# Kernel tuning notes

Hardware: AMD Instinct MI355X
Metric: run time of the kernel (lower is better)

Reference implementation:

```python
import jax, jax.numpy as jnp
import numpy as np

LN_EPS = 1e-5
N_NODES = 50000
IN_DIM = 128
OUT_DIM = 128
N_EDGES = 800000


def _ln(x, g, b):
    m = jnp.mean(x, axis=-1, keepdims=True)
    v = jnp.mean((x - m) ** 2, axis=-1, keepdims=True)
    return (x - m) * jax.lax.rsqrt(v + LN_EPS) * g + b


def setup_inputs() -> dict:
    key = jax.random.key(0)
    ks = jax.random.split(key, 16)

    def lin(k, fan_in, fan_out):
        return jax.random.normal(k, (fan_in, fan_out), dtype=jnp.float32) / np.sqrt(fan_in)

    x = jax.random.normal(ks[0], (N_NODES, IN_DIM), dtype=jnp.float32)
    edge_index = jax.random.randint(ks[1], (2, N_EDGES), 0, N_NODES, dtype=jnp.int64)
    return {
        "x": x,
        "edge_index": edge_index,
        # transform: Linear(in,out) + LayerNorm
        "W1": lin(ks[2], IN_DIM, OUT_DIM), "b1": jnp.zeros((OUT_DIM,), jnp.float32),
        "g1": jnp.ones((OUT_DIM,), jnp.float32), "bt1": jnp.zeros((OUT_DIM,), jnp.float32),
        # edge_attention: Linear(2*out,out) -> ReLU -> Linear(out,1) -> Sigmoid
        "We1": lin(ks[3], 2 * OUT_DIM, OUT_DIM), "be1": jnp.zeros((OUT_DIM,), jnp.float32),
        "We2": lin(ks[4], OUT_DIM, 1), "be2": jnp.zeros((1,), jnp.float32),
        # node_attention: Linear(out,out) -> ReLU -> Linear(out,1) -> Sigmoid (computed, unused)
        "Wn1": lin(ks[5], OUT_DIM, OUT_DIM), "bn1": jnp.zeros((OUT_DIM,), jnp.float32),
        "Wn2": lin(ks[6], OUT_DIM, 1), "bn2": jnp.zeros((1,), jnp.float32),
        # update_gate: Linear(2*out,out) -> Sigmoid
        "Wg": lin(ks[7], 2 * OUT_DIM, OUT_DIM), "bg": jnp.zeros((OUT_DIM,), jnp.float32),
        # final LayerNorm
        "g2": jnp.ones((OUT_DIM,), jnp.float32), "bt2": jnp.zeros((OUT_DIM,), jnp.float32),
    }


def reference(x, edge_index, W1, b1, g1, bt1, We1, be1, We2, be2,
              Wn1, bn1, Wn2, bn2, Wg, bg, g2, bt2):
    n = x.shape[0]
    # transform: Linear -> LayerNorm -> ReLU (Dropout is identity in eval)
    h = jax.nn.relu(_ln(x @ W1 + b1, g1, bt1))           # [N, D]
    row, col = edge_index[0], edge_index[1]
    h_src = h[row]                                        # [E, D]
    ef = jnp.concatenate([h_src, h[col]], axis=1)         # [E, 2D]
    edge_weights = jax.nn.sigmoid(jax.nn.relu(ef @ We1 + be1) @ We2 + be2)[:, 0]  # [E]
    # node_weights computed in original forward but never used in the output
    node_weights = jax.nn.sigmoid(jax.nn.relu(h @ Wn1 + bn1) @ Wn2 + bn2)[:, 0]
    _ = node_weights
    # weighted scatter-add: aggr[dst] += edge_weights[i] * h[src]
    aggr = jax.ops.segment_sum(edge_weights[:, None] * h_src, col, num_segments=n)  # [N, D]
    gate = jax.nn.sigmoid(jnp.concatenate([h, aggr], axis=-1) @ Wg + bg)
    h_new = gate * aggr + (1.0 - gate) * h
    return _ln(h_new, g2, bt2)
```

## Files before the change

kernel.cpp:

```cpp
#include <hip/hip_runtime.h>
#include <math.h>

#define D 128
#define NT 32
#define AGT 16
#define LP 132
#define SCB 64
#define HB 256

__device__ __forceinline__ float wave_allsum(float v) {
    #pragma unroll
    for (int off = 32; off; off >>= 1) v += __shfl_xor(v, off);
    return v;
}

__global__ void __launch_bounds__(256) fused_hist_transform(
    const int* __restrict__ ei, int* __restrict__ deg, int E,
    const float* __restrict__ x, const float* __restrict__ W1, const float* __restrict__ b1,
    const float* __restrict__ g1, const float* __restrict__ bt1,
    const float* __restrict__ We1, const float* __restrict__ be1,
    float* __restrict__ AH, float* __restrict__ B, int N)
{
    if (blockIdx.x < HB) {
        for (int e = blockIdx.x * 256 + threadIdx.x; e < E; e += HB * 256)
            atomicAdd(&deg[ei[E + e]], 1);
        return;
    }
    __shared__ float xs[NT][LP];
    const int t = threadIdx.x;
    const int q = t >> 6, lane = t & 63;
    const int cg = (lane & 31) * 4;
    const int kh = (lane >> 5) * 64;
    const int khi = lane >> 5;
    const int base = (blockIdx.x - HB) * NT;

    {
        int node = t >> 3, c0 = (t & 7) * 16;
        int gn = min(base + node, N - 1);
        const float4* src = (const float4*)(x + (size_t)gn * D + c0);
        float4* dst = (float4*)&xs[node][c0];
        dst[0] = src[0]; dst[1] = src[1]; dst[2] = src[2]; dst[3] = src[3];
    }

    float4 acc[8];
    #pragma unroll
    for (int n = 0; n < 8; ++n) acc[n] = make_float4(0.f,0.f,0.f,0.f);
    for (int k4 = 0; k4 < 16; ++k4) {
        int k = kh + k4 * 4;
        float4 w0 = *(const float4*)&W1[(k+0) * 128 + cg];
        float4 w1 = *(const float4*)&W1[(k+1) * 128 + cg];
        float4 w2 = *(const float4*)&W1[(k+2) * 128 + cg];
        float4 w3 = *(const float4*)&W1[(k+3) * 128 + cg];
        #pragma unroll
        for (int n = 0; n < 8; ++n) {
            float4 xv = *(const float4*)&xs[q*8+n][k];
            acc[n].x += xv.x*w0.x + xv.y*w1.x + xv.z*w2.x + xv.w*w3.x;
            acc[n].y += xv.x*w0.y + xv.y*w1.y + xv.z*w2.y + xv.w*w3.y;
            acc[n].z += xv.x*w0.z + xv.y*w1.z + xv.z*w2.z + xv.w*w3.z;
            acc[n].w += xv.x*w0.w + xv.y*w1.w + xv.z*w2.w + xv.w*w3.w;
        }
    }
    #pragma unroll
    for (int n = 0; n < 8; ++n) {
        acc[n].x += __shfl_xor(acc[n].x, 32);
        acc[n].y += __shfl_xor(acc[n].y, 32);
        acc[n].z += __shfl_xor(acc[n].z, 32);
        acc[n].w += __shfl_xor(acc[n].w, 32);
    }

    {
        float4 b4 = *(const float4*)&b1[cg];
        float4 g4 = *(const float4*)&g1[cg];
        float4 t4 = *(const float4*)&bt1[cg];
        #pragma unroll
        for (int n = 0; n < 8; ++n) {
            int node = q * 8 + n;
            float v0 = acc[n].x + b4.x, v1 = acc[n].y + b4.y;
            float v2 = acc[n].z + b4.z, v3 = acc[n].w + b4.w;
            float s  = wave_allsum(v0 + v1 + v2 + v3) * 0.5f;
            float qq = wave_allsum(v0*v0 + v1*v1 + v2*v2 + v3*v3) * 0.5f;
            float m = s * (1.f/128.f);
            float var = qq * (1.f/128.f) - m*m;
            float rs = rsqrtf(var + 1e-5f);
            float4 h4;
            h4.x = fmaxf((v0 - m)*rs*g4.x + t4.x, 0.f);
            h4.y = fmaxf((v1 - m)*rs*g4.y + t4.y, 0.f);
            h4.z = fmaxf((v2 - m)*rs*g4.z + t4.z, 0.f);
            h4.w = fmaxf((v3 - m)*rs*g4.w + t4.w, 0.f);
            if (khi == 0) {
                *(float4*)&xs[node][cg] = h4;
                int gn = base + node;
                if (gn < N) *(float4*)&AH[(size_t)gn * 256 + 128 + cg] = h4;
            }
        }
    }

    float4 aA[8], aB[8];
    #pragma unroll
    for (int n = 0; n < 8; ++n) { aA[n] = make_float4(0.f,0.f,0.f,0.f); aB[n] = make_float4(0.f,0.f,0.f,0.f); }
    for (int k4 = 0; k4 < 16; ++k4) {
        int k = kh + k4 * 4;
        float4 t0 = *(const float4*)&We1[(k+0) * 128 + cg];
        float4 t1 = *(const float4*)&We1[(k+1) * 128 + cg];
        float4 t2 = *(const float4*)&We1[(k+2) * 128 + cg];
        float4 t3 = *(const float4*)&We1[(k+3) * 128 + cg];
        float4 u0 = *(const float4*)&We1[(k+128) * 128 + cg];
        float4 u1 = *(const float4*)&We1[(k+129) * 128 + cg];
        float4 u2 = *(const float4*)&We1[(k+130) * 128 + cg];
        float4 u3 = *(const float4*)&We1[(k+131) * 128 + cg];
        #pragma unroll
        for (int n = 0; n < 8; ++n) {
            float4 hv = *(const float4*)&xs[q*8+n][k];
            aA[n].x += hv.x*t0.x + hv.y*t1.x + hv.z*t2.x + hv.w*t3.x;
            aA[n].y += hv.x*t0.y + hv.y*t1.y + hv.z*t2.y + hv.w*t3.y;
            aA[n].z += hv.x*t0.z + hv.y*t1.z + hv.z*t2.z + hv.w*t3.z;
            aA[n].w += hv.x*t0.w + hv.y*t1.w + hv.z*t2.w + hv.w*t3.w;
            aB[n].x += hv.x*u0.x + hv.y*u1.x + hv.z*u2.x + hv.w*u3.x;
            aB[n].y += hv.x*u0.y + hv.y*u1.y + hv.z*u2.y + hv.w*u3.y;
            aB[n].z += hv.x*u0.z + hv.y*u1.z + hv.z*u2.z + hv.w*u3.z;
            aB[n].w += hv.x*u0.w + hv.y*u1.w + hv.z*u2.w + hv.w*u3.w;
        }
    }
    {
        float4 be4 = *(const float4*)&be1[cg];
        #pragma unroll
        for (int n = 0; n < 8; ++n) {
            aA[n].x += __shfl_xor(aA[n].x, 32);
            aA[n].y += __shfl_xor(aA[n].y, 32);
            aA[n].z += __shfl_xor(aA[n].z, 32);
            aA[n].w += __shfl_xor(aA[n].w, 32);
            aB[n].x += __shfl_xor(aB[n].x, 32);
            aB[n].y += __shfl_xor(aB[n].y, 32);
            aB[n].z += __shfl_xor(aB[n].z, 32);
            aB[n].w += __shfl_xor(aB[n].w, 32);
            int gn = base + q*8 + n;
            if (khi == 0 && gn < N) {
                float4 a4 = make_float4(aA[n].x + be4.x, aA[n].y + be4.y,
                                        aA[n].z + be4.z, aA[n].w + be4.w);
                *(float4*)&AH[(size_t)gn * 256 + cg] = a4;
                *(float4*)&B[(size_t)gn * D + cg]    = aB[n];
            }
        }
    }
}

__global__ void __launch_bounds__(256) scan_a(const int* __restrict__ deg,
                                              int* __restrict__ bsum, int N) {
    __shared__ int red[256];
    const int b = blockIdx.x, t = threadIdx.x;
    const int C = (N + SCB - 1) / SCB;
    const int W = (C + 255) / 256;
    int s0 = b * C + t * W;
    int s1 = min(s0 + W, min((b + 1) * C, N));
    int s = 0;
    for (int i = s0; i < s1; ++i) s += deg[i];
    red[t] = s;
    __syncthreads();
    #pragma unroll
    for (int d = 128; d; d >>= 1) {
        if (t < d) red[t] += red[t + d];
        __syncthreads();
    }
    if (t == 0) bsum[b] = red[0];
}

__global__ void __launch_bounds__(256) scan_c(const int* __restrict__ deg,
                                              const int* __restrict__ bsum,
                                              int* __restrict__ off,
                                              int* __restrict__ cursor, int N) {
    __shared__ int pre[256];
    __shared__ int bofs;
    const int b = blockIdx.x, t = threadIdx.x;
    const int C = (N + SCB - 1) / SCB;
    const int W = (C + 255) / 256;
    if (t == 0) {
        int r = 0;
        for (int i = 0; i < b; ++i) r += bsum[i];
        bofs = r;
        if (b == SCB - 1) off[N] = r + bsum[b];
    }
    int s0 = b * C + t * W;
    int s1 = min(s0 + W, min((b + 1) * C, N));
    int s = 0;
    for (int i = s0; i < s1; ++i) s += deg[i];
    pre[t] = s;
    __syncthreads();
    for (int d = 1; d < 256; d <<= 1) {
        int vv = (t >= d) ? pre[t - d] : 0;
        __syncthreads();
        if (t >= d) pre[t] += vv;
        __syncthreads();
    }
    int run = bofs + ((t == 0) ? 0 : pre[t - 1]);
    for (int i = s0; i < s1; ++i) {
        off[i] = run;
        cursor[i] = run;
        run += deg[i];
    }
}

__global__ void __launch_bounds__(256) scatter_kernel(const int* __restrict__ ei,
                                                      int* __restrict__ cursor,
                                                      int* __restrict__ ssrc, int E) {
    int e = blockIdx.x * 256 + threadIdx.x;
    if (e < E) {
        int pos = atomicAdd(&cursor[ei[E + e]], 1);
        ssrc[pos] = ei[e];
    }
}

__global__ void __launch_bounds__(256) aggate(
    const int* __restrict__ off, const int* __restrict__ ssrc,
    const float* __restrict__ AH, const float* __restrict__ B,
    const float* __restrict__ We2, const float* __restrict__ be2,
    const float* __restrict__ Wg, const float* __restrict__ bg,
    const float* __restrict__ g2, const float* __restrict__ bt2,
    float* __restrict__ out, int N)
{
    __shared__ float hs[AGT][LP];
    __shared__ float ag[AGT][LP];
    const int t = threadIdx.x;
    const int q = t >> 6, lane = t & 63;
    const int g = lane >> 4;
    const int c8 = (lane & 15) * 8;
    const int base = blockIdx.x * AGT;

    {
        int node = t >> 4, c0 = (t & 15) * 8;
        size_t gofs = (size_t)min(base + node, N - 1) * 256 + 128 + c0;
        const float4* src = (const float4*)(AH + gofs);
        float4* dst = (float4*)&hs[node][c0];
        dst[0] = src[0]; dst[1] = src[1];
    }

    {
        const float4* Wp = (const float4*)(We2 + c8);
        float4 w0 = Wp[0], w1 = Wp[1];
        const float be = be2[0];

        for (int n = 0; n < 4; ++n) {
            int node = base + q * 4 + n;
            float4 acc0 = make_float4(0.f,0.f,0.f,0.f);
            float4 acc1 = make_float4(0.f,0.f,0.f,0.f);
            if (node < N) {
                const int s = off[node], e = off[node + 1];
                const int deg = e - s;
                if (deg > 0) {
                    const float4* Bp = (const float4*)(B + (size_t)node * D + c8);
                    float4 b0 = Bp[0], b1 = Bp[1];
                    if (deg <= 64) {
                        int myidx = ssrc[min(s + lane, e - 1)];
                        const int nit = (deg + 7) >> 3;
                        for (int it = 0; it < nit; ++it) {
                            int ja = it * 8 + g * 2;
                            int jb = ja + 1;
                            int sa = __shfl(myidx, min(ja, deg - 1));
                            int sb = __shfl(myidx, min(jb, deg - 1));
                            const float4* Ra = (const float4*)(AH + (size_t)sa * 256 + c8);
                            const float4* Rb = (const float4*)(AH + (size_t)sb * 256 + c8);
                            float4 aa0 = Ra[0], aa1 = Ra[1];
                            float4 ha0 = Ra[32], ha1 = Ra[33];
                            float4 ab0 = Rb[0], ab1 = Rb[1];
                            float4 hb0 = Rb[32], hb1 = Rb[33];
                            float da = fmaxf(aa0.x + b0.x, 0.f) * w0.x + fmaxf(aa0.y + b0.y, 0.f) * w0.y
                                     + fmaxf(aa0.z + b0.z, 0.f) * w0.z + fmaxf(aa0.w + b0.w, 0.f) * w0.w
                                     + fmaxf(aa1.x + b1.x, 0.f) * w1.x + fmaxf(aa1.y + b1.y, 0.f) * w1.y
                                     + fmaxf(aa1.z + b1.z, 0.f) * w1.z + fmaxf(aa1.w + b1.w, 0.f) * w1.w;
                            float db = fmaxf(ab0.x + b0.x, 0.f) * w0.x + fmaxf(ab0.y + b0.y, 0.f) * w0.y
                                     + fmaxf(ab0.z + b0.z, 0.f) * w0.z + fmaxf(ab0.w + b0.w, 0.f) * w0.w
                                     + fmaxf(ab1.x + b1.x, 0.f) * w1.x + fmaxf(ab1.y + b1.y, 0.f) * w1.y
                                     + fmaxf(ab1.z + b1.z, 0.f) * w1.z + fmaxf(ab1.w + b1.w, 0.f) * w1.w;
                            da += __shfl_xor(da, 1);  db += __shfl_xor(db, 1);
                            da += __shfl_xor(da, 2);  db += __shfl_xor(db, 2);
                            da += __shfl_xor(da, 4);  db += __shfl_xor(db, 4);
                            da += __shfl_xor(da, 8);  db += __shfl_xor(db, 8);
                            float wa = (ja < deg) ? 1.f / (1.f + expf(-(da + be))) : 0.f;
                            float wb = (jb < deg) ? 1.f / (1.f + expf(-(db + be))) : 0.f;
                            acc0.x += wa * ha0.x + wb * hb0.x; acc0.y += wa * ha0.y + wb * hb0.y;
                            acc0.z += wa * ha0.z + wb * hb0.z; acc0.w += wa * ha0.w + wb * hb0.w;
                            acc1.x += wa * ha1.x + wb * hb1.x; acc1.y += wa * ha1.y + wb * hb1.y;
                            acc1.z += wa * ha1.z + wb * hb1.z; acc1.w += wa * ha1.w + wb * hb1.w;
                        }
                    } else {
                        const int nit = (deg + 7) >> 3;
                        for (int it = 0; it < nit; ++it) {
                            int ja = s + it * 8 + g * 2;
                            int jb = ja + 1;
                            int sa = ssrc[min(ja, e - 1)];
                            int sb = ssrc[min(jb, e - 1)];
                            const float4* Ra = (const float4*)(AH + (size_t)sa * 256 + c8);
                            const float4* Rb = (const float4*)(AH + (size_t)sb * 256 + c8);
                            float4 aa0 = Ra[0], aa1 = Ra[1];
                            float4 ha0 = Ra[32], ha1 = Ra[33];
                            float4 ab0 = Rb[0], ab1 = Rb[1];
                            float4 hb0 = Rb[32], hb1 = Rb[33];
                            float da = fmaxf(aa0.x + b0.x, 0.f) * w0.x + fmaxf(aa0.y + b0.y, 0.f) * w0.y
                                     + fmaxf(aa0.z + b0.z, 0.f) * w0.z + fmaxf(aa0.w + b0.w, 0.f) * w0.w
                                     + fmaxf(aa1.x + b1.x, 0.f) * w1.x + fmaxf(aa1.y + b1.y, 0.f) * w1.y
                                     + fmaxf(aa1.z + b1.z, 0.f) * w1.z + fmaxf(aa1.w + b1.w, 0.f) * w1.w;
                            float db = fmaxf(ab0.x + b0.x, 0.f) * w0.x + fmaxf(ab0.y + b0.y, 0.f) * w0.y
                                     + fmaxf(ab0.z + b0.z, 0.f) * w0.z + fmaxf(ab0.w + b0.w, 0.f) * w0.w
                                     + fmaxf(ab1.x + b1.x, 0.f) * w1.x + fmaxf(ab1.y + b1.y, 0.f) * w1.y
                                     + fmaxf(ab1.z + b1.z, 0.f) * w1.z + fmaxf(ab1.w + b1.w, 0.f) * w1.w;
                            da += __shfl_xor(da, 1);  db += __shfl_xor(db, 1);
                            da += __shfl_xor(da, 2);  db += __shfl_xor(db, 2);
                            da += __shfl_xor(da, 4);  db += __shfl_xor(db, 4);
                            da += __shfl_xor(da, 8);  db += __shfl_xor(db, 8);
                            float wa = (ja < e) ? 1.f / (1.f + expf(-(da + be))) : 0.f;
                            float wb = (jb < e) ? 1.f / (1.f + expf(-(db + be))) : 0.f;
                            acc0.x += wa * ha0.x + wb * hb0.x; acc0.y += wa * ha0.y + wb * hb0.y;
                            acc0.z += wa * ha0.z + wb * hb0.z; acc0.w += wa * ha0.w + wb * hb0.w;
                            acc1.x += wa * ha1.x + wb * hb1.x; acc1.y += wa * ha1.y + wb * hb1.y;
                            acc1.z += wa * ha1.z + wb * hb1.z; acc1.w += wa * ha1.w + wb * hb1.w;
                        }
                    }
                    #pragma unroll
                    for (int o = 16; o <= 32; o <<= 1) {
                        acc0.x += __shfl_xor(acc0.x, o); acc0.y += __shfl_xor(acc0.y, o);
                        acc0.z += __shfl_xor(acc0.z, o); acc0.w += __shfl_xor(acc0.w, o);
                        acc1.x += __shfl_xor(acc1.x, o); acc1.y += __shfl_xor(acc1.y, o);
                        acc1.z += __shfl_xor(acc1.z, o); acc1.w += __shfl_xor(acc1.w, o);
                    }
                }
            }
            if (g == 0) {
                *(float4*)&ag[q*4+n][c8]     = acc0;
                *(float4*)&ag[q*4+n][c8 + 4] = acc1;
            }
        }
    }

    {
        const int cg = (lane & 31) * 4;
        const int kh = (lane >> 5) * 64;
        const int khi = lane >> 5;

        float4 acc[4];
        #pragma unroll
        for (int n = 0; n < 4; ++n) acc[n] = make_float4(0.f,0.f,0.f,0.f);
        for (int k4 = 0; k4 < 16; ++k4) {
            int k = kh + k4 * 4;
            float4 w0 = *(const float4*)&Wg[(k+0) * 128 + cg];
            float4 w1 = *(const float4*)&Wg[(k+1) * 128 + cg];
            float4 w2 = *(const float4*)&Wg[(k+2) * 128 + cg];
            float4 w3 = *(const float4*)&Wg[(k+3) * 128 + cg];
            float4 u0 = *(const float4*)&Wg[(k+128) * 128 + cg];
            float4 u1 = *(const float4*)&Wg[(k+129) * 128 + cg];
            float4 u2 = *(const float4*)&Wg[(k+130) * 128 + cg];
            float4 u3 = *(const float4*)&Wg[(k+131) * 128 + cg];
            #pragma unroll
            for (int n = 0; n < 4; ++n) {
                float4 v = *(const float4*)&hs[q*4+n][k];
                float4 a = *(const float4*)&ag[q*4+n][k];
                acc[n].x += v.x*w0.x + v.y*w1.x + v.z*w2.x + v.w*w3.x
                          + a.x*u0.x + a.y*u1.x + a.z*u2.x + a.w*u3.x;
                acc[n].y += v.x*w0.y + v.y*w1.y + v.z*w2.y + v.w*w3.y
                          + a.x*u0.y + a.y*u1.y + a.z*u2.y + a.w*u3.y;
                acc[n].z += v.x*w0.z + v.y*w1.z + v.z*w2.z + v.w*w3.z
                          + a.x*u0.z + a.y*u1.z + a.z*u2.z + a.w*u3.z;
                acc[n].w += v.x*w0.w + v.y*w1.w + v.z*w2.w + v.w*w3.w
                          + a.x*u0.w + a.y*u1.w + a.z*u2.w + a.w*u3.w;
            }
        }
        #pragma unroll
        for (int n = 0; n < 4; ++n) {
            acc[n].x += __shfl_xor(acc[n].x, 32);
            acc[n].y += __shfl_xor(acc[n].y, 32);
            acc[n].z += __shfl_xor(acc[n].z, 32);
            acc[n].w += __shfl_xor(acc[n].w, 32);
        }

        float4 bg4 = *(const float4*)&bg[cg];
        float4 gg4 = *(const float4*)&g2[cg];
        float4 bb4 = *(const float4*)&bt2[cg];
        #pragma unroll
        for (int n = 0; n < 4; ++n) {
            int node = q*4 + n;
            float4 av = *(const float4*)&ag[node][cg];
            float4 hv = *(const float4*)&hs[node][cg];
            float g0 = 1.f / (1.f + expf(-(acc[n].x + bg4.x)));
            float g1v = 1.f / (1.f + expf(-(acc[n].y + bg4.y)));
            float g2v = 1.f / (1.f + expf(-(acc[n].z + bg4.z)));
            float g3 = 1.f / (1.f + expf(-(acc[n].w + bg4.w)));
            float y0 = g0 * av.x + (1.f - g0) * hv.x;
            float y1 = g1v * av.y + (1.f - g1v) * hv.y;
            float y2 = g2v * av.z + (1.f - g2v) * hv.z;
            float y3 = g3 * av.w + (1.f - g3) * hv.w;
            float s  = wave_allsum(y0 + y1 + y2 + y3) * 0.5f;
            float qq = wave_allsum(y0*y0 + y1*y1 + y2*y2 + y3*y3) * 0.5f;
            float m = s * (1.f/128.f);
            float var = qq * (1.f/128.f) - m*m;
            float rs = rsqrtf(var + 1e-5f);
            int gn = base + node;
            if (khi == 0 && gn < N) {
                float4 o4;
                o4.x = (y0 - m)*rs*gg4.x + bb4.x;
                o4.y = (y1 - m)*rs*gg4.y + bb4.y;
                o4.z = (y2 - m)*rs*gg4.z + bb4.z;
                o4.w = (y3 - m)*rs*gg4.w + bb4.w;
                *(float4*)&out[(size_t)gn * D + cg] = o4;
            }
        }
    }
}

extern "C" void kernel_launch(void* const* d_in, const int* in_sizes, int n_in,
                              void* d_out, int out_size, void* d_ws, size_t ws_size,
                              hipStream_t stream) {
    const float* x   = (const float*)d_in[0];
    const int*   ei  = (const int*)d_in[1];
    const float* W1  = (const float*)d_in[2];
    const float* b1  = (const float*)d_in[3];
    const float* g1  = (const float*)d_in[4];
    const float* bt1 = (const float*)d_in[5];
    const float* We1 = (const float*)d_in[6];
    const float* be1 = (const float*)d_in[7];
    const float* We2 = (const float*)d_in[8];
    const float* be2 = (const float*)d_in[9];
    const float* Wg  = (const float*)d_in[14];
    const float* bg  = (const float*)d_in[15];
    const float* g2  = (const float*)d_in[16];
    const float* bt2 = (const float*)d_in[17];

    const int N = in_sizes[0] / D;
    const int E = in_sizes[1] / 2;
    const size_t ND = (size_t)N * D;

    float* AH   = (float*)d_ws;
    float* B    = AH + 2 * ND;
    int* deg    = (int*)(B + ND);
    int* off    = deg + (N + 1);
    int* cursor = off + (N + 1);
    int* ssrc   = cursor + (N + 1);
    int* bsum   = ssrc + E;

    (void)hipMemsetAsync(deg, 0, (size_t)(N + 1) * sizeof(int), stream);

    const int nblkT = (N + NT - 1) / NT;
    fused_hist_transform<<<HB + nblkT, 256, 0, stream>>>(
        ei, deg, E, x, W1, b1, g1, bt1, We1, be1, AH, B, N);
    scan_a<<<SCB, 256, 0, stream>>>(deg, bsum, N);
    scan_c<<<SCB, 256, 0, stream>>>(deg, bsum, off, cursor, N);
    scatter_kernel<<<(E + 255) / 256, 256, 0, stream>>>(ei, cursor, ssrc, E);
    aggate<<<(N + AGT - 1) / AGT, 256, 0, stream>>>(off, ssrc, AH, B, We2, be2,
                                                    Wg, bg, g2, bt2, (float*)d_out, N);
}
```

Baseline: 335.1 us.

## Fuse CSR build into transform kernel using in-kernel grid barriers

Merges the degree histogram, the two-pass scan and the edge scatter into the first 64 blocks of the transform kernel, synchronized by atomic counter spin barriers. This removes three kernel launches and lets CSR construction overlap with the dense transform work running in the other blocks. The cost is fewer blocks (64 instead of 256) doing the histogram and scatter atomics, plus spin-wait barriers. Those barriers assume all 64 CSR blocks are co-resident, which holds because they have the lowest block indices.

```diff
diff --git a/kernel.cpp b/kernel.cpp
--- a/kernel.cpp
+++ b/kernel.cpp
@@ -5,8 +5,7 @@
 #define NT 32
 #define AGT 16
 #define LP 132
-#define SCB 64
-#define HB 256
+#define CSB 64
 
 __device__ __forceinline__ float wave_allsum(float v) {
     #pragma unroll
@@ -14,25 +13,95 @@
     return v;
 }
 
-__global__ void __launch_bounds__(256) fused_hist_transform(
-    const int* __restrict__ ei, int* __restrict__ deg, int E,
+__global__ void __launch_bounds__(256) fused_csr_transform(
+    const int* __restrict__ ei, int* __restrict__ deg, int* __restrict__ ctr,
+    int* __restrict__ bsum, int* __restrict__ off, int* __restrict__ cursor,
+    int* __restrict__ ssrc, int E,
     const float* __restrict__ x, const float* __restrict__ W1, const float* __restrict__ b1,
     const float* __restrict__ g1, const float* __restrict__ bt1,
     const float* __restrict__ We1, const float* __restrict__ be1,
     float* __restrict__ AH, float* __restrict__ B, int N)
 {
-    if (blockIdx.x < HB) {
-        for (int e = blockIdx.x * 256 + threadIdx.x; e < E; e += HB * 256)
+    if (blockIdx.x < CSB) {
+        __shared__ int red[256];
+        __shared__ int bofs;
+        const int b = blockIdx.x, t = threadIdx.x;
+
+        for (int e = b * 256 + t; e < E; e += CSB * 256)
             atomicAdd(&deg[ei[E + e]], 1);
+        __threadfence();
+        __syncthreads();
+        if (t == 0) {
+            atomicAdd(&ctr[0], 1);
+            while (atomicAdd(&ctr[0], 0) < CSB) __builtin_amdgcn_s_sleep(2);
+        }
+        __syncthreads();
+
+        const int C = (N + CSB - 1) / CSB;
+        const int W = (C + 255) / 256;
+        int s0 = b * C + t * W;
+        int s1 = min(s0 + W, min((b + 1) * C, N));
+        int s = 0;
+        for (int i = s0; i < s1; ++i) s += atomicAdd(&deg[i], 0);
+        red[t] = s;
+        __syncthreads();
+        #pragma unroll
+        for (int d = 128; d; d >>= 1) {
+            if (t < d) red[t] += red[t + d];
+            __syncthreads();
+        }
+        if (t == 0) atomicExch(&bsum[b], red[0]);
+        __threadfence();
+        __syncthreads();
+        if (t == 0) {
+            atomicAdd(&ctr[1], 1);
+            while (atomicAdd(&ctr[1], 0) < CSB) __builtin_amdgcn_s_sleep(2);
+        }
+        __syncthreads();
+
+        if (t == 0) {
+            int r = 0;
+            for (int i = 0; i < b; ++i) r += atomicAdd(&bsum[i], 0);
+            bofs = r;
+            if (b == CSB - 1) atomicExch(&off[N], r + atomicAdd(&bsum[b], 0));
+        }
+        red[t] = s;
+        __syncthreads();
+        for (int d = 1; d < 256; d <<= 1) {
+            int vv = (t >= d) ? red[t - d] : 0;
+            __syncthreads();
+            if (t >= d) red[t] += vv;
+            __syncthreads();
+        }
+        int run = bofs + ((t == 0) ? 0 : red[t - 1]);
+        for (int i = s0; i < s1; ++i) {
+            int dv = atomicAdd(&deg[i], 0);
+            atomicExch(&off[i], run);
+            atomicExch(&cursor[i], run);
+            run += dv;
+        }
+        __threadfence();
+        __syncthreads();
+        if (t == 0) {
+            atomicAdd(&ctr[2], 1);
+            while (atomicAdd(&ctr[2], 0) < CSB) __builtin_amdgcn_s_sleep(2);
+        }
+        __syncthreads();
+
+        for (int e = b * 256 + t; e < E; e += CSB * 256) {
+            int pos = atomicAdd(&cursor[ei[E + e]], 1);
+            ssrc[pos] = ei[e];
+        }
         return;
     }
+
     __shared__ float xs[NT][LP];
     const int t = threadIdx.x;
     const int q = t >> 6, lane = t & 63;
     const int cg = (lane & 31) * 4;
     const int kh = (lane >> 5) * 64;
     const int khi = lane >> 5;
-    const int base = (blockIdx.x - HB) * NT;
+    const int base = (blockIdx.x - CSB) * NT;
 
     {
         int node = t >> 3, c0 = (t & 7) * 16;
@@ -141,71 +210,6 @@
                 *(float4*)&B[(size_t)gn * D + cg]    = aB[n];
             }
         }
-    }
-}
-
-__global__ void __launch_bounds__(256) scan_a(const int* __restrict__ deg,
-                                              int* __restrict__ bsum, int N) {
-    __shared__ int red[256];
-    const int b = blockIdx.x, t = threadIdx.x;
-    const int C = (N + SCB - 1) / SCB;
-    const int W = (C + 255) / 256;
-    int s0 = b * C + t * W;
-    int s1 = min(s0 + W, min((b + 1) * C, N));
-    int s = 0;
-    for (int i = s0; i < s1; ++i) s += deg[i];
-    red[t] = s;
-    __syncthreads();
-    #pragma unroll
-    for (int d = 128; d; d >>= 1) {
-        if (t < d) red[t] += red[t + d];
-        __syncthreads();
-    }
-    if (t == 0) bsum[b] = red[0];
-}
-
-__global__ void __launch_bounds__(256) scan_c(const int* __restrict__ deg,
-                                              const int* __restrict__ bsum,
-                                              int* __restrict__ off,
-                                              int* __restrict__ cursor, int N) {
-    __shared__ int pre[256];
-    __shared__ int bofs;
-    const int b = blockIdx.x, t = threadIdx.x;
-    const int C = (N + SCB - 1) / SCB;
-    const int W = (C + 255) / 256;
-    if (t == 0) {
-        int r = 0;
-        for (int i = 0; i < b; ++i) r += bsum[i];
-        bofs = r;
-        if (b == SCB - 1) off[N] = r + bsum[b];
-    }
-    int s0 = b * C + t * W;
-    int s1 = min(s0 + W, min((b + 1) * C, N));
-    int s = 0;
-    for (int i = s0; i < s1; ++i) s += deg[i];
-    pre[t] = s;
-    __syncthreads();
-    for (int d = 1; d < 256; d <<= 1) {
-        int vv = (t >= d) ? pre[t - d] : 0;
-        __syncthreads();
-        if (t >= d) pre[t] += vv;
-        __syncthreads();
-    }
-    int run = bofs + ((t == 0) ? 0 : pre[t - 1]);
-    for (int i = s0; i < s1; ++i) {
-        off[i] = run;
-        cursor[i] = run;
-        run += deg[i];
-    }
-}
-
-__global__ void __launch_bounds__(256) scatter_kernel(const int* __restrict__ ei,
-                                                      int* __restrict__ cursor,
-                                                      int* __restrict__ ssrc, int E) {
-    int e = blockIdx.x * 256 + threadIdx.x;
-    if (e < E) {
-        int pos = atomicAdd(&cursor[ei[E + e]], 1);
-        ssrc[pos] = ei[e];
     }
 }
 
@@ -429,19 +433,18 @@
     float* AH   = (float*)d_ws;
     float* B    = AH + 2 * ND;
     int* deg    = (int*)(B + ND);
-    int* off    = deg + (N + 1);
+    int* ctr    = deg + (N + 1);
+    int* off    = ctr + 8;
     int* cursor = off + (N + 1);
     int* ssrc   = cursor + (N + 1);
     int* bsum   = ssrc + E;
 
-    (void)hipMemsetAsync(deg, 0, (size_t)(N + 1) * sizeof(int), stream);
+    (void)hipMemsetAsync(deg, 0, (size_t)(N + 1 + 8) * sizeof(int), stream);
 
     const int nblkT = (N + NT - 1) / NT;
-    fused_hist_transform<<<HB + nblkT, 256, 0, stream>>>(
-        ei, deg, E, x, W1, b1, g1, bt1, We1, be1, AH, B, N);
-    scan_a<<<SCB, 256, 0, stream>>>(deg, bsum, N);
-    scan_c<<<SCB, 256, 0, stream>>>(deg, bsum, off, cursor, N);
-    scatter_kernel<<<(E + 255) / 256, 256, 0, stream>>>(ei, cursor, ssrc, E);
+    fused_csr_transform<<<CSB + nblkT, 256, 0, stream>>>(
+        ei, deg, ctr, bsum, off, cursor, ssrc, E,
+        x, W1, b1, g1, bt1, We1, be1, AH, B, N);
     aggate<<<(N + AGT - 1) / AGT, 256, 0, stream>>>(off, ssrc, AH, B, We2, be2,
                                                     Wg, bg, g2, bt2, (float*)d_out, N);
 }
```

Result: faster. 310.6 us (-7.3%).
